# Kernel tuning notes

Measured on AMD Instinct MI355X. Metric: run time of the kernel, lower is better.

## Reference

```python
import jax, jax.numpy as jnp
import numpy as np

D_MODEL = 128
DEPTH = 4
LN_EPS = 1e-5


def _ssm(x, Wi, A, Wo):
    # x: [B, L, D]; Wi: [3D, D]; A: [D]; Wo: [D, D]
    z = jnp.einsum('bld,ed->ble', x, Wi)          # [B, L, 3D]
    u, i, o = jnp.split(z, 3, axis=-1)
    iu = jax.nn.sigmoid(i) * jnp.tanh(u)          # gated input, [B, L, D]
    og = jax.nn.sigmoid(o)                        # output gate
    a = jnp.minimum(jnp.exp(A), 0.999)            # decay, [D]

    def step(s, c):
        s = a * s + c
        return s, s

    s0 = jnp.zeros((x.shape[0], x.shape[2]), x.dtype)
    _, S = jax.lax.scan(step, s0, jnp.swapaxes(iu, 0, 1))  # [L, B, D]
    y = og * jnp.swapaxes(S, 0, 1)                # [B, L, D]
    return jnp.einsum('bld,ed->ble', y, Wo)


def _scan_2d(x, Wi, A, Wo):
    # x: [N, D, H, W] -> four directional 1D scans, averaged
    N, D, H, W = x.shape
    xh = jnp.transpose(x, (0, 2, 3, 1))           # [N, H, W, D]
    lr = _ssm(xh.reshape(N * H, W, D), Wi, A, Wo).reshape(N, H, W, D)
    rl = _ssm(jnp.flip(xh, 2).reshape(N * H, W, D), Wi, A, Wo).reshape(N, H, W, D)
    rl = jnp.flip(rl, 2)
    xw = jnp.transpose(x, (0, 3, 2, 1))           # [N, W, H, D]
    ud = _ssm(xw.reshape(N * W, H, D), Wi, A, Wo).reshape(N, W, H, D)
    du = _ssm(jnp.flip(xw, 2).reshape(N * W, H, D), Wi, A, Wo).reshape(N, W, H, D)
    du = jnp.flip(du, 2)
    y = (lr + rl + jnp.transpose(ud, (0, 2, 1, 3)) + jnp.transpose(du, (0, 2, 1, 3))) / 4
    return jnp.transpose(y, (0, 3, 1, 2))         # [N, D, H, W]


def setup_inputs() -> dict:
    key = jax.random.key(0)
    ks = jax.random.split(key, 8)
    D = D_MODEL
    lin = 1.0 / np.sqrt(D)
    tok = jax.random.normal(ks[0], (8, 16, D, 32, 32), jnp.float32)
    s_inp = jax.random.normal(ks[1], (DEPTH, 3 * D, D), jnp.float32) * lin
    s_A = jax.random.normal(ks[2], (DEPTH, D), jnp.float32) * -0.1
    s_out = jax.random.normal(ks[3], (DEPTH, D, D), jnp.float32) * lin
    t_inp = jax.random.normal(ks[4], (DEPTH, 3 * D, D), jnp.float32) * lin
    t_A = jax.random.normal(ks[5], (DEPTH, D), jnp.float32) * -0.1
    t_out = jax.random.normal(ks[6], (DEPTH, D, D), jnp.float32) * lin
    ln_g = jnp.ones((D,), jnp.float32)
    ln_b = jnp.zeros((D,), jnp.float32)
    return {"tok": tok, "s_inp": s_inp, "s_A": s_A, "s_out": s_out,
            "t_inp": t_inp, "t_A": t_A, "t_out": t_out,
            "ln_g": ln_g, "ln_b": ln_b}


def reference(tok, s_inp, s_A, s_out, t_inp, t_A, t_out, ln_g, ln_b):
    B, T, D, h, w = tok.shape
    x = tok
    for l in range(DEPTH):
        xs = x.reshape(B * T, D, h, w)
        xs = _scan_2d(xs, s_inp[l], s_A[l], s_out[l]).reshape(B, T, D, h, w)
        xt = jnp.transpose(xs, (0, 3, 4, 1, 2)).reshape(B * h * w, T, D)
        xt = _ssm(xt, t_inp[l], t_A[l], t_out[l]).reshape(B, h, w, T, D)
        x = x + jnp.transpose(xt, (0, 3, 4, 1, 2))
    xn = jnp.transpose(x, (0, 1, 3, 4, 2))        # [B,T,h,w,D]
    mu = jnp.mean(xn, axis=-1, keepdims=True)
    var = jnp.var(xn, axis=-1, keepdims=True)
    xn = (xn - mu) / jnp.sqrt(var + LN_EPS) * ln_g + ln_b
    return jnp.transpose(xn, (0, 1, 4, 2, 3))     # [B,T,D,h,w]
```

## Files before the change

kernel.cpp:

```cpp
#include <hip/hip_runtime.h>
#include <hip/hip_bf16.h>
#include <math.h>

#define D_MODEL 128
#define HW      1024
#define DEPTH   4
#define NIMG    128
#define B_      8
#define T_      16
#define LN_EPSF 1e-5f

typedef short  s8  __attribute__((ext_vector_type(8)));
typedef ushort us8 __attribute__((ext_vector_type(8)));
typedef ushort us4 __attribute__((ext_vector_type(4)));
typedef float  f4  __attribute__((ext_vector_type(4)));

__device__ __forceinline__ float sig_(float x) { return 1.0f / (1.0f + __expf(-x)); }
__device__ __forceinline__ float tanh_(float x) { return 2.0f * sig_(2.0f * x) - 1.0f; }
__device__ __forceinline__ ushort f2b(float f) {
    __hip_bfloat16 h = __float2bfloat16(f);
    return *reinterpret_cast<ushort*>(&h);
}
__device__ __forceinline__ float b2f(ushort u) {
    __hip_bfloat16 h = *reinterpret_cast<__hip_bfloat16*>(&u);
    return __bfloat162float(h);
}

__global__ __launch_bounds__(256) void wconv_kernel(
    const float* __restrict__ src, ushort* __restrict__ dst, int n)
{
    int i = blockIdx.x * 256 + threadIdx.x;
    if (i < n) dst[i] = f2b(src[i]);
}

__device__ __forceinline__ void gates_from_lds(
    const ushort (*Xs)[136], const ushort* __restrict__ Wi,
    ushort* __restrict__ iu, ushort* __restrict__ og,
    size_t nbase, int q0, int tid)
{
    const int lane = tid & 63;
    const int wv   = tid >> 6;
    const int grp  = lane >> 4;
    const int lrow = lane & 15;
    const int ch0  = wv * 32;

    f4 aU[2][4], aI[2][4], aO[2][4];
    #pragma unroll
    for (int nt = 0; nt < 2; ++nt)
        #pragma unroll
        for (int qt = 0; qt < 4; ++qt) { aU[nt][qt] = (f4)0.f; aI[nt][qt] = (f4)0.f; aO[nt][qt] = (f4)0.f; }

    #pragma unroll
    for (int kk = 0; kk < 4; ++kk) {
        const int kb = kk * 32 + grp * 8;
        s8 xb[4], wu[2], wi[2], wo[2];
        #pragma unroll
        for (int qt = 0; qt < 4; ++qt)
            xb[qt] = *reinterpret_cast<const s8*>(&Xs[qt * 16 + lrow][kb]);
        #pragma unroll
        for (int nt = 0; nt < 2; ++nt) {
            const int e = ch0 + nt * 16 + lrow;
            wu[nt] = *reinterpret_cast<const s8*>(Wi + (size_t)e * D_MODEL + kb);
            wi[nt] = *reinterpret_cast<const s8*>(Wi + (size_t)(e + 128) * D_MODEL + kb);
            wo[nt] = *reinterpret_cast<const s8*>(Wi + (size_t)(e + 256) * D_MODEL + kb);
        }
        #pragma unroll
        for (int nt = 0; nt < 2; ++nt)
            #pragma unroll
            for (int qt = 0; qt < 4; ++qt) {
                aU[nt][qt] = __builtin_amdgcn_mfma_f32_16x16x32_bf16(wu[nt], xb[qt], aU[nt][qt], 0, 0, 0);
                aI[nt][qt] = __builtin_amdgcn_mfma_f32_16x16x32_bf16(wi[nt], xb[qt], aI[nt][qt], 0, 0, 0);
                aO[nt][qt] = __builtin_amdgcn_mfma_f32_16x16x32_bf16(wo[nt], xb[qt], aO[nt][qt], 0, 0, 0);
            }
    }

    #pragma unroll
    for (int nt = 0; nt < 2; ++nt)
        #pragma unroll
        for (int qt = 0; qt < 4; ++qt) {
            const int q = q0 + qt * 16 + lrow;
            const size_t off = nbase + (size_t)q * D_MODEL + ch0 + nt * 16 + grp * 4;
            us4 piu, pog;
            #pragma unroll
            for (int i = 0; i < 4; ++i) {
                piu[i] = f2b(sig_(aI[nt][qt][i]) * tanh_(aU[nt][qt][i]));
                pog[i] = f2b(sig_(aO[nt][qt][i]));
            }
            *reinterpret_cast<us4*>(iu + off) = piu;
            *reinterpret_cast<us4*>(og + off) = pog;
        }
}

__device__ __forceinline__ void stage1_gfrags(
    const ushort* __restrict__ S, const ushort* __restrict__ og,
    float scale, size_t nbase, int q0, int wv, int grp, int lrow, s8 g[4])
{
    const size_t rbase = nbase + (size_t)(q0 + wv * 16 + lrow) * D_MODEL + grp * 8;
    #pragma unroll
    for (int kk = 0; kk < 4; ++kk) {
        const size_t off = rbase + kk * 32;
        us8 sv = *reinterpret_cast<const us8*>(S + off);
        us8 ov = *reinterpret_cast<const us8*>(og + off);
        s8 gg;
        #pragma unroll
        for (int j = 0; j < 8; ++j)
            gg[j] = (short)f2b(b2f(sv[j]) * b2f(ov[j]) * scale);
        g[kk] = gg;
    }
}

__global__ __launch_bounds__(256, 2) void gates_f32_kernel(
    const float* __restrict__ in, const ushort* __restrict__ Wi,
    ushort* __restrict__ iu, ushort* __restrict__ og)
{
    __shared__ ushort Xs[64][136];
    const int n   = blockIdx.x >> 4;
    const int q0  = (blockIdx.x & 15) << 6;
    const int tid = threadIdx.x;
    const size_t nbase = (size_t)n * (D_MODEL * HW);

    {
        const float* inb = in + nbase + q0;
        const int q   = tid & 63;
        const int dh0 = tid >> 6;
        for (int it = 0; it < 4; ++it) {
            const int dh = dh0 + it * 4;
            s8 pk;
            #pragma unroll
            for (int j = 0; j < 8; ++j)
                pk[j] = (short)f2b(inb[(size_t)(dh * 8 + j) * HW + q]);
            *reinterpret_cast<s8*>(&Xs[q][dh * 8]) = pk;
        }
    }
    __syncthreads();
    gates_from_lds(Xs, Wi, iu, og, nbase, q0, tid);
}

__global__ __launch_bounds__(256, 2) void fusedA_kernel(
    const ushort* __restrict__ S, const ushort* __restrict__ og_in,
    const ushort* __restrict__ Wo, const ushort* __restrict__ Wi2,
    ushort* __restrict__ iu, ushort* __restrict__ og, float scale)
{
    __shared__ ushort Xs[64][136];
    const int n   = blockIdx.x >> 4;
    const int q0  = (blockIdx.x & 15) << 6;
    const int tid = threadIdx.x;
    const int lane = tid & 63, wv = tid >> 6, grp = lane >> 4, lrow = lane & 15;
    const size_t nbase = (size_t)n * (D_MODEL * HW);

    s8 g[4];
    stage1_gfrags(S, og_in, scale, nbase, q0, wv, grp, lrow, g);

    f4 C[8];
    #pragma unroll
    for (int et = 0; et < 8; ++et) C[et] = (f4)0.f;
    #pragma unroll
    for (int kk = 0; kk < 4; ++kk) {
        const int kb = kk * 32 + grp * 8;
        #pragma unroll
        for (int et = 0; et < 8; ++et) {
            s8 wf = *reinterpret_cast<const s8*>(Wo + (size_t)(et * 16 + lrow) * D_MODEL + kb);
            C[et] = __builtin_amdgcn_mfma_f32_16x16x32_bf16(g[kk], wf, C[et], 0, 0, 0);
        }
    }

    #pragma unroll
    for (int et = 0; et < 8; ++et)
        #pragma unroll
        for (int i = 0; i < 4; ++i)
            Xs[wv * 16 + grp * 4 + i][et * 16 + lrow] = f2b(C[et][i]);
    __syncthreads();

    gates_from_lds(Xs, Wi2, iu, og, nbase, q0, tid);
}

template <bool GATES, bool LN>
__global__ __launch_bounds__(256, 2) void fusedB_kernel(
    const ushort* __restrict__ S, const ushort* __restrict__ og_in,
    const ushort* __restrict__ Wo, const float* __restrict__ resid,
    float* __restrict__ X, const ushort* __restrict__ Wi2,
    ushort* __restrict__ iu, ushort* __restrict__ og,
    const float* __restrict__ lng, const float* __restrict__ lnb)
{
    __shared__ ushort Xs[64][136];
    const int n   = blockIdx.x >> 4;
    const int q0  = (blockIdx.x & 15) << 6;
    const int tid = threadIdx.x;
    const int lane = tid & 63, wv = tid >> 6, grp = lane >> 4, lrow = lane & 15;
    const size_t nbase = (size_t)n * (D_MODEL * HW);

    s8 g[4];
    stage1_gfrags(S, og_in, 1.0f, nbase, q0, wv, grp, lrow, g);

    f4 C[8];
    #pragma unroll
    for (int et = 0; et < 8; ++et) C[et] = (f4)0.f;
    #pragma unroll
    for (int kk = 0; kk < 4; ++kk) {
        const int kb = kk * 32 + grp * 8;
        #pragma unroll
        for (int et = 0; et < 8; ++et) {
            s8 wf = *reinterpret_cast<const s8*>(Wo + (size_t)(et * 16 + lrow) * D_MODEL + kb);
            C[et] = __builtin_amdgcn_mfma_f32_16x16x32_bf16(g[kk], wf, C[et], 0, 0, 0);
        }
    }

    const int qb = q0 + wv * 16 + grp * 4;

    if constexpr (LN) {
        float sum[4] = {0.f, 0.f, 0.f, 0.f}, sq[4] = {0.f, 0.f, 0.f, 0.f};
        #pragma unroll
        for (int et = 0; et < 8; ++et) {
            const int e = et * 16 + lrow;
            const size_t off = nbase + (size_t)e * HW + qb;
            f4 r = *reinterpret_cast<const f4*>(resid + off);
            #pragma unroll
            for (int i = 0; i < 4; ++i) {
                float v = C[et][i] + r[i];
                C[et][i] = v;
                sum[i] += v; sq[i] += v * v;
            }
        }
        #pragma unroll
        for (int m = 1; m <= 8; m <<= 1)
            #pragma unroll
            for (int i = 0; i < 4; ++i) {
                sum[i] += __shfl_xor(sum[i], m);
                sq[i]  += __shfl_xor(sq[i], m);
            }
        float mean[4], rstd[4];
        #pragma unroll
        for (int i = 0; i < 4; ++i) {
            mean[i] = sum[i] * (1.f / D_MODEL);
            float var = sq[i] * (1.f / D_MODEL) - mean[i] * mean[i];
            rstd[i] = rsqrtf(var + LN_EPSF);
        }
        #pragma unroll
        for (int et = 0; et < 8; ++et) {
            const int e = et * 16 + lrow;
            const float ge = lng[e], be = lnb[e];
            const size_t off = nbase + (size_t)e * HW + qb;
            f4 o;
            #pragma unroll
            for (int i = 0; i < 4; ++i)
                o[i] = (C[et][i] - mean[i]) * rstd[i] * ge + be;
            *reinterpret_cast<f4*>(X + off) = o;
        }
    } else {
        #pragma unroll
        for (int et = 0; et < 8; ++et) {
            const int e = et * 16 + lrow;
            const size_t off = nbase + (size_t)e * HW + qb;
            f4 r = *reinterpret_cast<const f4*>(resid + off);
            f4 v;
            #pragma unroll
            for (int i = 0; i < 4; ++i) v[i] = C[et][i] + r[i];
            *reinterpret_cast<f4*>(X + off) = v;
            if constexpr (GATES) {
                #pragma unroll
                for (int i = 0; i < 4; ++i)
                    Xs[wv * 16 + grp * 4 + i][e] = f2b(v[i]);
            }
        }
        if constexpr (GATES) {
            __syncthreads();
            gates_from_lds(Xs, Wi2, iu, og, nbase, q0, tid);
        }
    }
}

__global__ __launch_bounds__(256) void rowscan_kernel(
    const ushort* __restrict__ iu, ushort* __restrict__ R,
    const float* __restrict__ Av)
{
    const int tid = blockIdx.x * 256 + threadIdx.x;
    const int d = tid & 127;
    const int i = (tid >> 7) & 31;
    const int n = tid >> 12;
    const float a = fminf(__expf(Av[d]), 0.999f);
    const size_t base = (size_t)n * (D_MODEL * HW) + (size_t)(i * 32) * D_MODEL + d;

    float x[32], acc[32];
    #pragma unroll
    for (int j = 0; j < 32; ++j) x[j] = b2f(iu[base + (size_t)j * D_MODEL]);
    float s = 0.f;
    #pragma unroll
    for (int j = 0; j < 32; ++j) { s = fmaf(a, s, x[j]); acc[j] = s; }
    s = 0.f;
    #pragma unroll
    for (int j = 31; j >= 0; --j) { s = fmaf(a, s, x[j]); acc[j] += s; }
    #pragma unroll
    for (int j = 0; j < 32; ++j) R[base + (size_t)j * D_MODEL] = f2b(acc[j]);
}

__global__ __launch_bounds__(256) void colscan_kernel(
    ushort* __restrict__ buf, const ushort* __restrict__ R,
    const float* __restrict__ Av)
{
    const int tid = blockIdx.x * 256 + threadIdx.x;
    const int d = tid & 127;
    const int j = (tid >> 7) & 31;
    const int n = tid >> 12;
    const float a = fminf(__expf(Av[d]), 0.999f);
    const size_t base = (size_t)n * (D_MODEL * HW) + (size_t)j * D_MODEL + d;
    const size_t istr = (size_t)32 * D_MODEL;

    float x[32], t[32];
    #pragma unroll
    for (int i = 0; i < 32; ++i) x[i] = b2f(buf[base + i * istr]);
    float s = 0.f;
    #pragma unroll
    for (int i = 0; i < 32; ++i) { s = fmaf(a, s, x[i]); t[i] = s; }
    s = 0.f;
    #pragma unroll
    for (int i = 31; i >= 0; --i) { s = fmaf(a, s, x[i]); t[i] += s; }
    #pragma unroll
    for (int i = 0; i < 32; ++i)
        buf[base + i * istr] = f2b(t[i] + b2f(R[base + i * istr]));
}

__global__ __launch_bounds__(256) void tscan_kernel(
    ushort* __restrict__ buf, const float* __restrict__ Av)
{
    const int tid = blockIdx.x * 256 + threadIdx.x;
    const int dc = tid & 15;
    const int q  = (tid >> 4) & 1023;
    const int b  = tid >> 14;
    float aa[8], st[8];
    #pragma unroll
    for (int jj = 0; jj < 8; ++jj) {
        aa[jj] = fminf(__expf(Av[dc * 8 + jj]), 0.999f);
        st[jj] = 0.f;
    }
    #pragma unroll
    for (int t = 0; t < T_; ++t) {
        const size_t off = ((size_t)(b * T_ + t) * HW + q) * D_MODEL + dc * 8;
        us8 v = *reinterpret_cast<us8*>(buf + off);
        us8 w;
        #pragma unroll
        for (int jj = 0; jj < 8; ++jj) {
            st[jj] = fmaf(aa[jj], st[jj], b2f(v[jj]));
            w[jj] = f2b(st[jj]);
        }
        *reinterpret_cast<us8*>(buf + off) = w;
    }
}

extern "C" void kernel_launch(void* const* d_in, const int* in_sizes, int n_in,
                              void* d_out, int out_size, void* d_ws, size_t ws_size,
                              hipStream_t stream) {
    const float* tok   = (const float*)d_in[0];
    const float* s_inp = (const float*)d_in[1];
    const float* s_A   = (const float*)d_in[2];
    const float* s_out = (const float*)d_in[3];
    const float* t_inp = (const float*)d_in[4];
    const float* t_A   = (const float*)d_in[5];
    const float* t_out = (const float*)d_in[6];
    const float* ln_g  = (const float*)d_in[7];
    const float* ln_b  = (const float*)d_in[8];

    float*  X    = (float*)d_out;
    ushort* Abuf = (ushort*)d_ws;
    ushort* Bbuf = Abuf + (size_t)16777216;
    ushort* Cbuf = Bbuf + (size_t)16777216;
    ushort* Wbf  = Cbuf + (size_t)16777216;
    ushort* sWiB = Wbf;
    ushort* sWoB = Wbf + 196608;
    ushort* tWiB = Wbf + 262144;
    ushort* tWoB = Wbf + 458752;

    const dim3 blk256(256);

    wconv_kernel<<<768, blk256, 0, stream>>>(s_inp, sWiB, 196608);
    wconv_kernel<<<256, blk256, 0, stream>>>(s_out, sWoB, 65536);
    wconv_kernel<<<768, blk256, 0, stream>>>(t_inp, tWiB, 196608);
    wconv_kernel<<<256, blk256, 0, stream>>>(t_out, tWoB, 65536);

    gates_f32_kernel<<<2048, blk256, 0, stream>>>(tok, sWiB, Abuf, Bbuf);

    for (int l = 0; l < DEPTH; ++l) {
        const float* xin = (l == 0) ? tok : X;

        rowscan_kernel<<<2048, blk256, 0, stream>>>(Abuf, Cbuf, s_A + (size_t)l * 128);
        colscan_kernel<<<2048, blk256, 0, stream>>>(Abuf, Cbuf, s_A + (size_t)l * 128);
        fusedA_kernel<<<2048, blk256, 0, stream>>>(
            Abuf, Bbuf, sWoB + (size_t)l * 16384, tWiB + (size_t)l * 49152,
            Abuf, Bbuf, 0.25f);
        tscan_kernel<<<512, blk256, 0, stream>>>(Abuf, t_A + (size_t)l * 128);

        if (l < DEPTH - 1) {
            fusedB_kernel<true, false><<<2048, blk256, 0, stream>>>(
                Abuf, Bbuf, tWoB + (size_t)l * 16384, xin, X,
                sWiB + (size_t)(l + 1) * 49152, Abuf, Bbuf, nullptr, nullptr);
        } else {
            fusedB_kernel<false, true><<<2048, blk256, 0, stream>>>(
                Abuf, Bbuf, tWoB + (size_t)l * 16384, xin, X,
                nullptr, nullptr, nullptr, ln_g, ln_b);
        }
    }
}
```

Baseline: 850.8 us.

## Fuse 2D scans into one LDS kernel and fold temporal scan into mega kernel

```diff
diff --git a/kernel.cpp b/kernel.cpp
--- a/kernel.cpp
+++ b/kernel.cpp
@@ -9,11 +9,15 @@
 #define B_      8
 #define T_      16
 #define LN_EPSF 1e-5f
+#define TLN     131072
+#define PS      1033
 
 typedef short  s8  __attribute__((ext_vector_type(8)));
 typedef ushort us8 __attribute__((ext_vector_type(8)));
 typedef ushort us4 __attribute__((ext_vector_type(4)));
 typedef float  f4  __attribute__((ext_vector_type(4)));
+
+#define MFMA __builtin_amdgcn_mfma_f32_16x16x32_bf16
 
 __device__ __forceinline__ float sig_(float x) { return 1.0f / (1.0f + __expf(-x)); }
 __device__ __forceinline__ float tanh_(float x) { return 2.0f * sig_(2.0f * x) - 1.0f; }
@@ -33,16 +37,13 @@
     if (i < n) dst[i] = f2b(src[i]);
 }
 
-__device__ __forceinline__ void gates_from_lds(
+__device__ __forceinline__ void gates_from_lds_TL(
     const ushort (*Xs)[136], const ushort* __restrict__ Wi,
     ushort* __restrict__ iu, ushort* __restrict__ og,
     size_t nbase, int q0, int tid)
 {
-    const int lane = tid & 63;
-    const int wv   = tid >> 6;
-    const int grp  = lane >> 4;
-    const int lrow = lane & 15;
-    const int ch0  = wv * 32;
+    const int lane = tid & 63, wv = tid >> 6, grp = lane >> 4, lrow = lane & 15;
+    const int ch0 = wv * 32;
 
     f4 aU[2][4], aI[2][4], aO[2][4];
     #pragma unroll
@@ -68,9 +69,9 @@
         for (int nt = 0; nt < 2; ++nt)
             #pragma unroll
             for (int qt = 0; qt < 4; ++qt) {
-                aU[nt][qt] = __builtin_amdgcn_mfma_f32_16x16x32_bf16(wu[nt], xb[qt], aU[nt][qt], 0, 0, 0);
-                aI[nt][qt] = __builtin_amdgcn_mfma_f32_16x16x32_bf16(wi[nt], xb[qt], aI[nt][qt], 0, 0, 0);
-                aO[nt][qt] = __builtin_amdgcn_mfma_f32_16x16x32_bf16(wo[nt], xb[qt], aO[nt][qt], 0, 0, 0);
+                aU[nt][qt] = MFMA(wu[nt], xb[qt], aU[nt][qt], 0, 0, 0);
+                aI[nt][qt] = MFMA(wi[nt], xb[qt], aI[nt][qt], 0, 0, 0);
+                aO[nt][qt] = MFMA(wo[nt], xb[qt], aO[nt][qt], 0, 0, 0);
             }
     }
 
@@ -78,8 +79,9 @@
     for (int nt = 0; nt < 2; ++nt)
         #pragma unroll
         for (int qt = 0; qt < 4; ++qt) {
-            const int q = q0 + qt * 16 + lrow;
-            const size_t off = nbase + (size_t)q * D_MODEL + ch0 + nt * 16 + grp * 4;
+            const int ch = ch0 + nt * 16 + grp * 4;
+            const int q  = q0 + qt * 16 + lrow;
+            const size_t off = nbase + (size_t)(ch >> 3) * 8192 + (size_t)q * 8 + (ch & 7);
             us4 piu, pog;
             #pragma unroll
             for (int i = 0; i < 4; ++i) {
@@ -89,24 +91,6 @@
             *reinterpret_cast<us4*>(iu + off) = piu;
             *reinterpret_cast<us4*>(og + off) = pog;
         }
-}
-
-__device__ __forceinline__ void stage1_gfrags(
-    const ushort* __restrict__ S, const ushort* __restrict__ og,
-    float scale, size_t nbase, int q0, int wv, int grp, int lrow, s8 g[4])
-{
-    const size_t rbase = nbase + (size_t)(q0 + wv * 16 + lrow) * D_MODEL + grp * 8;
-    #pragma unroll
-    for (int kk = 0; kk < 4; ++kk) {
-        const size_t off = rbase + kk * 32;
-        us8 sv = *reinterpret_cast<const us8*>(S + off);
-        us8 ov = *reinterpret_cast<const us8*>(og + off);
-        s8 gg;
-        #pragma unroll
-        for (int j = 0; j < 8; ++j)
-            gg[j] = (short)f2b(b2f(sv[j]) * b2f(ov[j]) * scale);
-        g[kk] = gg;
-    }
 }
 
 __global__ __launch_bounds__(256, 2) void gates_f32_kernel(
@@ -117,12 +101,11 @@
     const int n   = blockIdx.x >> 4;
     const int q0  = (blockIdx.x & 15) << 6;
     const int tid = threadIdx.x;
-    const size_t nbase = (size_t)n * (D_MODEL * HW);
+    const size_t nbase = (size_t)n * TLN;
 
     {
         const float* inb = in + nbase + q0;
-        const int q   = tid & 63;
-        const int dh0 = tid >> 6;
+        const int q = tid & 63, dh0 = tid >> 6;
         for (int it = 0; it < 4; ++it) {
             const int dh = dh0 + it * 4;
             s8 pk;
@@ -133,216 +116,286 @@
         }
     }
     __syncthreads();
-    gates_from_lds(Xs, Wi, iu, og, nbase, q0, tid);
-}
-
-__global__ __launch_bounds__(256, 2) void fusedA_kernel(
-    const ushort* __restrict__ S, const ushort* __restrict__ og_in,
-    const ushort* __restrict__ Wo, const ushort* __restrict__ Wi2,
-    ushort* __restrict__ iu, ushort* __restrict__ og, float scale)
+    gates_from_lds_TL(Xs, Wi, iu, og, nbase, q0, tid);
+}
+
+__global__ __launch_bounds__(256, 2) void scan2d_kernel(
+    ushort* bufG , const ushort* __restrict__ og,
+    const float* __restrict__ Av)
 {
-    __shared__ ushort Xs[64][136];
+    __shared__ float P[8 * PS];
+    __shared__ float R[8 * PS];
     const int n   = blockIdx.x >> 4;
-    const int q0  = (blockIdx.x & 15) << 6;
+    const int oct = blockIdx.x & 15;
     const int tid = threadIdx.x;
-    const int lane = tid & 63, wv = tid >> 6, grp = lane >> 4, lrow = lane & 15;
-    const size_t nbase = (size_t)n * (D_MODEL * HW);
-
-    s8 g[4];
-    stage1_gfrags(S, og_in, scale, nbase, q0, wv, grp, lrow, g);
-
-    f4 C[8];
-    #pragma unroll
-    for (int et = 0; et < 8; ++et) C[et] = (f4)0.f;
-    #pragma unroll
-    for (int kk = 0; kk < 4; ++kk) {
-        const int kb = kk * 32 + grp * 8;
-        #pragma unroll
-        for (int et = 0; et < 8; ++et) {
-            s8 wf = *reinterpret_cast<const s8*>(Wo + (size_t)(et * 16 + lrow) * D_MODEL + kb);
-            C[et] = __builtin_amdgcn_mfma_f32_16x16x32_bf16(g[kk], wf, C[et], 0, 0, 0);
-        }
-    }
-
-    #pragma unroll
-    for (int et = 0; et < 8; ++et)
-        #pragma unroll
-        for (int i = 0; i < 4; ++i)
-            Xs[wv * 16 + grp * 4 + i][et * 16 + lrow] = f2b(C[et][i]);
+    const size_t base = (size_t)n * TLN + (size_t)oct * 8192;
+
+    for (int it = 0; it < 4; ++it) {
+        const int p  = it * 256 + tid;
+        const int sw = p ^ (((p >> 5) & 7) << 2);
+        us8 v = *reinterpret_cast<const us8*>(bufG + base + (size_t)p * 8);
+        #pragma unroll
+        for (int dc = 0; dc < 8; ++dc) P[dc * PS + sw] = b2f(v[dc]);
+    }
     __syncthreads();
 
-    gates_from_lds(Xs, Wi2, iu, og, nbase, q0, tid);
-}
-
-template <bool GATES, bool LN>
-__global__ __launch_bounds__(256, 2) void fusedB_kernel(
-    const ushort* __restrict__ S, const ushort* __restrict__ og_in,
-    const ushort* __restrict__ Wo, const float* __restrict__ resid,
-    float* __restrict__ X, const ushort* __restrict__ Wi2,
-    ushort* __restrict__ iu, ushort* __restrict__ og,
+    const int dc  = tid & 7;
+    const int row = tid >> 3;
+    const float a = fminf(__expf(Av[oct * 8 + dc]), 0.999f);
+
+    {
+        const int swb = (row * 32) ^ (((row & 7) << 2));
+        float x[32], r[32];
+        #pragma unroll
+        for (int j = 0; j < 32; ++j) x[j] = P[dc * PS + (swb ^ j)];
+        float s = 0.f;
+        #pragma unroll
+        for (int j = 0; j < 32; ++j) { s = fmaf(a, s, x[j]); r[j] = s; }
+        s = 0.f;
+        #pragma unroll
+        for (int j = 31; j >= 0; --j) { s = fmaf(a, s, x[j]); r[j] += s; }
+        #pragma unroll
+        for (int j = 0; j < 32; ++j) R[dc * PS + (swb ^ j)] = r[j];
+    }
+    __syncthreads();
+
+    {
+        float x[32], t[32];
+        #pragma unroll
+        for (int i = 0; i < 32; ++i) {
+            const int p = i * 32 + row;
+            x[i] = P[dc * PS + (p ^ ((i & 7) << 2))];
+        }
+        float s = 0.f;
+        #pragma unroll
+        for (int i = 0; i < 32; ++i) { s = fmaf(a, s, x[i]); t[i] = s; }
+        s = 0.f;
+        #pragma unroll
+        for (int i = 31; i >= 0; --i) { s = fmaf(a, s, x[i]); t[i] += s; }
+        #pragma unroll
+        for (int i = 0; i < 32; ++i) {
+            const int idx = dc * PS + ((i * 32 + row) ^ ((i & 7) << 2));
+            P[idx] = t[i] + R[idx];
+        }
+    }
+    __syncthreads();
+
+    for (int it = 0; it < 4; ++it) {
+        const int p  = it * 256 + tid;
+        const int sw = p ^ (((p >> 5) & 7) << 2);
+        us8 o = *reinterpret_cast<const us8*>(og + base + (size_t)p * 8);
+        us8 w;
+        #pragma unroll
+        for (int d2 = 0; d2 < 8; ++d2)
+            w[d2] = f2b(b2f(o[d2]) * P[d2 * PS + sw] * 0.25f);
+        *reinterpret_cast<us8*>(bufG + base + (size_t)p * 8) = w;
+    }
+}
+
+template <int MODE>
+__global__ __launch_bounds__(256, 2) void mega_kernel(
+    ushort* bufA , ushort* bufB ,
+    const ushort* __restrict__ WoS, const ushort* __restrict__ WiT,
+    const float* __restrict__ AvT,  const ushort* __restrict__ WoT,
+    const float* __restrict__ resid, float* __restrict__ X,
+    const ushort* __restrict__ WiS2,
     const float* __restrict__ lng, const float* __restrict__ lnb)
 {
-    __shared__ ushort Xs[64][136];
-    const int n   = blockIdx.x >> 4;
-    const int q0  = (blockIdx.x & 15) << 6;
-    const int tid = threadIdx.x;
+    __shared__ ushort Ls0[16][136];
+    __shared__ ushort Ls1[16][136];
+    __shared__ float  LnP[2][4][16];
+
+    const int b    = blockIdx.x >> 6;
+    const int qb0  = (blockIdx.x & 63) << 4;
+    const int tid  = threadIdx.x;
     const int lane = tid & 63, wv = tid >> 6, grp = lane >> 4, lrow = lane & 15;
-    const size_t nbase = (size_t)n * (D_MODEL * HW);
-
-    s8 g[4];
-    stage1_gfrags(S, og_in, 1.0f, nbase, q0, wv, grp, lrow, g);
-
-    f4 C[8];
-    #pragma unroll
-    for (int et = 0; et < 8; ++et) C[et] = (f4)0.f;
-    #pragma unroll
-    for (int kk = 0; kk < 4; ++kk) {
-        const int kb = kk * 32 + grp * 8;
-        #pragma unroll
-        for (int et = 0; et < 8; ++et) {
-            s8 wf = *reinterpret_cast<const s8*>(Wo + (size_t)(et * 16 + lrow) * D_MODEL + kb);
-            C[et] = __builtin_amdgcn_mfma_f32_16x16x32_bf16(g[kk], wf, C[et], 0, 0, 0);
-        }
-    }
-
-    const int qb = q0 + wv * 16 + grp * 4;
-
-    if constexpr (LN) {
-        float sum[4] = {0.f, 0.f, 0.f, 0.f}, sq[4] = {0.f, 0.f, 0.f, 0.f};
-        #pragma unroll
-        for (int et = 0; et < 8; ++et) {
-            const int e = et * 16 + lrow;
-            const size_t off = nbase + (size_t)e * HW + qb;
-            f4 r = *reinterpret_cast<const f4*>(resid + off);
+    const int c_oct = tid >> 4, c_qq = tid & 15;
+
+    float aT[2];
+    aT[0] = fminf(__expf(AvT[wv * 32 + lrow]), 0.999f);
+    aT[1] = fminf(__expf(AvT[wv * 32 + 16 + lrow]), 0.999f);
+    float ge[2], be[2];
+    if constexpr (MODE == 1) {
+        ge[0] = lng[wv * 32 + lrow];      be[0] = lnb[wv * 32 + lrow];
+        ge[1] = lng[wv * 32 + 16 + lrow]; be[1] = lnb[wv * 32 + 16 + lrow];
+    }
+
+    f4 st[2]; st[0] = (f4)0.f; st[1] = (f4)0.f;
+
+    us8 gpre = *reinterpret_cast<const us8*>(
+        bufA + (size_t)(b * T_) * TLN + (size_t)c_oct * 8192 + (size_t)(qb0 + c_qq) * 8);
+
+    for (int t = 0; t < T_; ++t) {
+        const int n = b * T_ + t;
+        const size_t nbase = (size_t)n * TLN;
+
+        *reinterpret_cast<us8*>(&Ls0[c_qq][c_oct * 8]) = gpre;
+        __syncthreads();
+        if (t + 1 < T_)
+            gpre = *reinterpret_cast<const us8*>(
+                bufA + (size_t)(n + 1) * TLN + (size_t)c_oct * 8192 + (size_t)(qb0 + c_qq) * 8);
+
+        s8 gf[4];
+        #pragma unroll
+        for (int kk = 0; kk < 4; ++kk)
+            gf[kk] = *reinterpret_cast<const s8*>(&Ls0[lrow][kk * 32 + grp * 8]);
+        f4 c1[2]; c1[0] = (f4)0.f; c1[1] = (f4)0.f;
+        #pragma unroll
+        for (int kk = 0; kk < 4; ++kk) {
+            const int kb = kk * 32 + grp * 8;
+            #pragma unroll
+            for (int nt = 0; nt < 2; ++nt) {
+                s8 wf = *reinterpret_cast<const s8*>(WoS + (size_t)(wv * 32 + nt * 16 + lrow) * D_MODEL + kb);
+                c1[nt] = MFMA(gf[kk], wf, c1[nt], 0, 0, 0);
+            }
+        }
+        #pragma unroll
+        for (int nt = 0; nt < 2; ++nt)
+            #pragma unroll
+            for (int i = 0; i < 4; ++i)
+                Ls1[grp * 4 + i][wv * 32 + nt * 16 + lrow] = f2b(c1[nt][i]);
+        __syncthreads();
+
+        s8 xf[4];
+        #pragma unroll
+        for (int kk = 0; kk < 4; ++kk)
+            xf[kk] = *reinterpret_cast<const s8*>(&Ls1[lrow][kk * 32 + grp * 8]);
+        f4 aU[2], aI[2], aO[2];
+        #pragma unroll
+        for (int nt = 0; nt < 2; ++nt) { aU[nt] = (f4)0.f; aI[nt] = (f4)0.f; aO[nt] = (f4)0.f; }
+        #pragma unroll
+        for (int kk = 0; kk < 4; ++kk) {
+            const int kb = kk * 32 + grp * 8;
+            #pragma unroll
+            for (int nt = 0; nt < 2; ++nt) {
+                const int e = wv * 32 + nt * 16 + lrow;
+                s8 wu = *reinterpret_cast<const s8*>(WiT + (size_t)e * D_MODEL + kb);
+                s8 wi = *reinterpret_cast<const s8*>(WiT + (size_t)(e + 128) * D_MODEL + kb);
+                s8 wo = *reinterpret_cast<const s8*>(WiT + (size_t)(e + 256) * D_MODEL + kb);
+                aU[nt] = MFMA(xf[kk], wu, aU[nt], 0, 0, 0);
+                aI[nt] = MFMA(xf[kk], wi, aI[nt], 0, 0, 0);
+                aO[nt] = MFMA(xf[kk], wo, aO[nt], 0, 0, 0);
+            }
+        }
+        #pragma unroll
+        for (int nt = 0; nt < 2; ++nt)
             #pragma unroll
             for (int i = 0; i < 4; ++i) {
-                float v = C[et][i] + r[i];
-                C[et][i] = v;
-                sum[i] += v; sq[i] += v * v;
-            }
-        }
-        #pragma unroll
-        for (int m = 1; m <= 8; m <<= 1)
+                const float iuv = sig_(aI[nt][i]) * tanh_(aU[nt][i]);
+                st[nt][i] = fmaf(aT[nt], st[nt][i], iuv);
+                Ls0[grp * 4 + i][wv * 32 + nt * 16 + lrow] = f2b(sig_(aO[nt][i]) * st[nt][i]);
+            }
+        __syncthreads();
+
+        s8 g2f[4];
+        #pragma unroll
+        for (int kk = 0; kk < 4; ++kk)
+            g2f[kk] = *reinterpret_cast<const s8*>(&Ls0[lrow][kk * 32 + grp * 8]);
+        f4 c3[2]; c3[0] = (f4)0.f; c3[1] = (f4)0.f;
+        #pragma unroll
+        for (int kk = 0; kk < 4; ++kk) {
+            const int kb = kk * 32 + grp * 8;
+            #pragma unroll
+            for (int nt = 0; nt < 2; ++nt) {
+                s8 wf = *reinterpret_cast<const s8*>(WoT + (size_t)(wv * 32 + nt * 16 + lrow) * D_MODEL + kb);
+                c3[nt] = MFMA(g2f[kk], wf, c3[nt], 0, 0, 0);
+            }
+        }
+        f4 v[2];
+        #pragma unroll
+        for (int nt = 0; nt < 2; ++nt) {
+            const int e = wv * 32 + nt * 16 + lrow;
+            const size_t offX = nbase + (size_t)e * HW + (qb0 + grp * 4);
+            f4 r = *reinterpret_cast<const f4*>(resid + offX);
+            #pragma unroll
+            for (int i = 0; i < 4; ++i) v[nt][i] = c3[nt][i] + r[i];
+            if constexpr (MODE == 0)
+                *reinterpret_cast<f4*>(X + offX) = v[nt];
+        }
+
+        if constexpr (MODE == 0) {
+            #pragma unroll
+            for (int nt = 0; nt < 2; ++nt)
+                #pragma unroll
+                for (int i = 0; i < 4; ++i)
+                    Ls1[grp * 4 + i][wv * 32 + nt * 16 + lrow] = f2b(v[nt][i]);
+            __syncthreads();
+            s8 xb2[4];
+            #pragma unroll
+            for (int kk = 0; kk < 4; ++kk)
+                xb2[kk] = *reinterpret_cast<const s8*>(&Ls1[lrow][kk * 32 + grp * 8]);
+            f4 bU[2], bI[2], bO[2];
+            #pragma unroll
+            for (int nt = 0; nt < 2; ++nt) { bU[nt] = (f4)0.f; bI[nt] = (f4)0.f; bO[nt] = (f4)0.f; }
+            #pragma unroll
+            for (int kk = 0; kk < 4; ++kk) {
+                const int kb = kk * 32 + grp * 8;
+                #pragma unroll
+                for (int nt = 0; nt < 2; ++nt) {
+                    const int ch = wv * 32 + nt * 16 + lrow;
+                    s8 wu = *reinterpret_cast<const s8*>(WiS2 + (size_t)ch * D_MODEL + kb);
+                    s8 wi = *reinterpret_cast<const s8*>(WiS2 + (size_t)(ch + 128) * D_MODEL + kb);
+                    s8 wo = *reinterpret_cast<const s8*>(WiS2 + (size_t)(ch + 256) * D_MODEL + kb);
+                    bU[nt] = MFMA(wu, xb2[kk], bU[nt], 0, 0, 0);
+                    bI[nt] = MFMA(wi, xb2[kk], bI[nt], 0, 0, 0);
+                    bO[nt] = MFMA(wo, xb2[kk], bO[nt], 0, 0, 0);
+                }
+            }
+            #pragma unroll
+            for (int nt = 0; nt < 2; ++nt) {
+                const int ch = wv * 32 + nt * 16 + grp * 4;
+                const int q  = qb0 + lrow;
+                const size_t off = nbase + (size_t)(ch >> 3) * 8192 + (size_t)q * 8 + (ch & 7);
+                us4 piu, pog;
+                #pragma unroll
+                for (int i = 0; i < 4; ++i) {
+                    piu[i] = f2b(sig_(bI[nt][i]) * tanh_(bU[nt][i]));
+                    pog[i] = f2b(sig_(bO[nt][i]));
+                }
+                *reinterpret_cast<us4*>(bufA + off) = piu;
+                *reinterpret_cast<us4*>(bufB + off) = pog;
+            }
+        } else {
+            float s4[4], q4[4];
             #pragma unroll
             for (int i = 0; i < 4; ++i) {
-                sum[i] += __shfl_xor(sum[i], m);
-                sq[i]  += __shfl_xor(sq[i], m);
-            }
-        float mean[4], rstd[4];
-        #pragma unroll
-        for (int i = 0; i < 4; ++i) {
-            mean[i] = sum[i] * (1.f / D_MODEL);
-            float var = sq[i] * (1.f / D_MODEL) - mean[i] * mean[i];
-            rstd[i] = rsqrtf(var + LN_EPSF);
-        }
-        #pragma unroll
-        for (int et = 0; et < 8; ++et) {
-            const int e = et * 16 + lrow;
-            const float ge = lng[e], be = lnb[e];
-            const size_t off = nbase + (size_t)e * HW + qb;
-            f4 o;
-            #pragma unroll
-            for (int i = 0; i < 4; ++i)
-                o[i] = (C[et][i] - mean[i]) * rstd[i] * ge + be;
-            *reinterpret_cast<f4*>(X + off) = o;
-        }
-    } else {
-        #pragma unroll
-        for (int et = 0; et < 8; ++et) {
-            const int e = et * 16 + lrow;
-            const size_t off = nbase + (size_t)e * HW + qb;
-            f4 r = *reinterpret_cast<const f4*>(resid + off);
-            f4 v;
-            #pragma unroll
-            for (int i = 0; i < 4; ++i) v[i] = C[et][i] + r[i];
-            *reinterpret_cast<f4*>(X + off) = v;
-            if constexpr (GATES) {
+                s4[i] = v[0][i] + v[1][i];
+                q4[i] = v[0][i] * v[0][i] + v[1][i] * v[1][i];
+            }
+            #pragma unroll
+            for (int m = 1; m <= 8; m <<= 1)
+                #pragma unroll
+                for (int i = 0; i < 4; ++i) {
+                    s4[i] += __shfl_xor(s4[i], m);
+                    q4[i] += __shfl_xor(q4[i], m);
+                }
+            if (lrow == 0)
+                #pragma unroll
+                for (int i = 0; i < 4; ++i) {
+                    LnP[0][wv][grp * 4 + i] = s4[i];
+                    LnP[1][wv][grp * 4 + i] = q4[i];
+                }
+            __syncthreads();
+            float mean[4], rstd[4];
+            #pragma unroll
+            for (int i = 0; i < 4; ++i) {
+                float S = 0.f, Q = 0.f;
+                #pragma unroll
+                for (int w = 0; w < 4; ++w) { S += LnP[0][w][grp * 4 + i]; Q += LnP[1][w][grp * 4 + i]; }
+                mean[i] = S * (1.f / D_MODEL);
+                rstd[i] = rsqrtf(Q * (1.f / D_MODEL) - mean[i] * mean[i] + LN_EPSF);
+            }
+            #pragma unroll
+            for (int nt = 0; nt < 2; ++nt) {
+                const int e = wv * 32 + nt * 16 + lrow;
+                const size_t offX = nbase + (size_t)e * HW + (qb0 + grp * 4);
+                f4 o;
                 #pragma unroll
                 for (int i = 0; i < 4; ++i)
-                    Xs[wv * 16 + grp * 4 + i][e] = f2b(v[i]);
-            }
-        }
-        if constexpr (GATES) {
-            __syncthreads();
-            gates_from_lds(Xs, Wi2, iu, og, nbase, q0, tid);
-        }
-    }
-}
-
-__global__ __launch_bounds__(256) void rowscan_kernel(
-    const ushort* __restrict__ iu, ushort* __restrict__ R,
-    const float* __restrict__ Av)
-{
-    const int tid = blockIdx.x * 256 + threadIdx.x;
-    const int d = tid & 127;
-    const int i = (tid >> 7) & 31;
-    const int n = tid >> 12;
-    const float a = fminf(__expf(Av[d]), 0.999f);
-    const size_t base = (size_t)n * (D_MODEL * HW) + (size_t)(i * 32) * D_MODEL + d;
-
-    float x[32], acc[32];
-    #pragma unroll
-    for (int j = 0; j < 32; ++j) x[j] = b2f(iu[base + (size_t)j * D_MODEL]);
-    float s = 0.f;
-    #pragma unroll
-    for (int j = 0; j < 32; ++j) { s = fmaf(a, s, x[j]); acc[j] = s; }
-    s = 0.f;
-    #pragma unroll
-    for (int j = 31; j >= 0; --j) { s = fmaf(a, s, x[j]); acc[j] += s; }
-    #pragma unroll
-    for (int j = 0; j < 32; ++j) R[base + (size_t)j * D_MODEL] = f2b(acc[j]);
-}
-
-__global__ __launch_bounds__(256) void colscan_kernel(
-    ushort* __restrict__ buf, const ushort* __restrict__ R,
-    const float* __restrict__ Av)
-{
-    const int tid = blockIdx.x * 256 + threadIdx.x;
-    const int d = tid & 127;
-    const int j = (tid >> 7) & 31;
-    const int n = tid >> 12;
-    const float a = fminf(__expf(Av[d]), 0.999f);
-    const size_t base = (size_t)n * (D_MODEL * HW) + (size_t)j * D_MODEL + d;
-    const size_t istr = (size_t)32 * D_MODEL;
-
-    float x[32], t[32];
-    #pragma unroll
-    for (int i = 0; i < 32; ++i) x[i] = b2f(buf[base + i * istr]);
-    float s = 0.f;
-    #pragma unroll
-    for (int i = 0; i < 32; ++i) { s = fmaf(a, s, x[i]); t[i] = s; }
-    s = 0.f;
-    #pragma unroll
-    for (int i = 31; i >= 0; --i) { s = fmaf(a, s, x[i]); t[i] += s; }
-    #pragma unroll
-    for (int i = 0; i < 32; ++i)
-        buf[base + i * istr] = f2b(t[i] + b2f(R[base + i * istr]));
-}
-
-__global__ __launch_bounds__(256) void tscan_kernel(
-    ushort* __restrict__ buf, const float* __restrict__ Av)
-{
-    const int tid = blockIdx.x * 256 + threadIdx.x;
-    const int dc = tid & 15;
-    const int q  = (tid >> 4) & 1023;
-    const int b  = tid >> 14;
-    float aa[8], st[8];
-    #pragma unroll
-    for (int jj = 0; jj < 8; ++jj) {
-        aa[jj] = fminf(__expf(Av[dc * 8 + jj]), 0.999f);
-        st[jj] = 0.f;
-    }
-    #pragma unroll
-    for (int t = 0; t < T_; ++t) {
-        const size_t off = ((size_t)(b * T_ + t) * HW + q) * D_MODEL + dc * 8;
-        us8 v = *reinterpret_cast<us8*>(buf + off);
-        us8 w;
-        #pragma unroll
-        for (int jj = 0; jj < 8; ++jj) {
-            st[jj] = fmaf(aa[jj], st[jj], b2f(v[jj]));
-            w[jj] = f2b(st[jj]);
-        }
-        *reinterpret_cast<us8*>(buf + off) = w;
+                    o[i] = (v[nt][i] - mean[i]) * rstd[i] * ge[nt] + be[nt];
+                *reinterpret_cast<f4*>(X + offX) = o;
+            }
+        }
     }
 }
 
@@ -362,8 +415,7 @@
     float*  X    = (float*)d_out;
     ushort* Abuf = (ushort*)d_ws;
     ushort* Bbuf = Abuf + (size_t)16777216;
-    ushort* Cbuf = Bbuf + (size_t)16777216;
-    ushort* Wbf  = Cbuf + (size_t)16777216;
+    ushort* Wbf  = Bbuf + (size_t)16777216;
     ushort* sWiB = Wbf;
     ushort* sWoB = Wbf + 196608;
     ushort* tWiB = Wbf + 262144;
@@ -381,21 +433,20 @@
     for (int l = 0; l < DEPTH; ++l) {
         const float* xin = (l == 0) ? tok : X;
 
-        rowscan_kernel<<<2048, blk256, 0, stream>>>(Abuf, Cbuf, s_A + (size_t)l * 128);
-        colscan_kernel<<<2048, blk256, 0, stream>>>(Abuf, Cbuf, s_A + (size_t)l * 128);
-        fusedA_kernel<<<2048, blk256, 0, stream>>>(
-            Abuf, Bbuf, sWoB + (size_t)l * 16384, tWiB + (size_t)l * 49152,
-            Abuf, Bbuf, 0.25f);
-        tscan_kernel<<<512, blk256, 0, stream>>>(Abuf, t_A + (size_t)l * 128);
+        scan2d_kernel<<<2048, blk256, 0, stream>>>(Abuf, Bbuf, s_A + (size_t)l * 128);
 
         if (l < DEPTH - 1) {
-            fusedB_kernel<true, false><<<2048, blk256, 0, stream>>>(
-                Abuf, Bbuf, tWoB + (size_t)l * 16384, xin, X,
-                sWiB + (size_t)(l + 1) * 49152, Abuf, Bbuf, nullptr, nullptr);
+            mega_kernel<0><<<512, blk256, 0, stream>>>(
+                Abuf, Bbuf,
+                sWoB + (size_t)l * 16384, tWiB + (size_t)l * 49152,
+                t_A + (size_t)l * 128, tWoB + (size_t)l * 16384,
+                xin, X, sWiB + (size_t)(l + 1) * 49152, nullptr, nullptr);
         } else {
-            fusedB_kernel<false, true><<<2048, blk256, 0, stream>>>(
-                Abuf, Bbuf, tWoB + (size_t)l * 16384, xin, X,
-                nullptr, nullptr, nullptr, ln_g, ln_b);
-        }
-    }
-}
+            mega_kernel<1><<<512, blk256, 0, stream>>>(
+                Abuf, Bbuf,
+                sWoB + (size_t)l * 16384, tWiB + (size_t)l * 49152,
+                t_A + (size_t)l * 128, tWoB + (size_t)l * 16384,
+                xin, X, nullptr, ln_g, ln_b);
+        }
+    }
+}
```

After: 711.8 us. 1.2x faster.
